# Optimization experiments

Hardware: AMD Instinct MI355X
Metric: run time of the kernel (lower is better)

Reference implementation:

```python
import math
import jax, jax.numpy as jnp
import numpy as np

N_NODES = 100000
N_EDGES = 1600000
IN_DIM, HID_DIM, OUT_DIM = 8, 64, 112


def _glorot(key, fan_in, fan_out):
    lim = math.sqrt(6.0 / (fan_in + fan_out))
    return jax.random.uniform(key, (fan_in, fan_out), jnp.float32, -lim, lim)


def _layer_params(key, in_d, out_d):
    ks = jax.random.split(key, 8)
    return dict(
        Wq=_glorot(ks[0], in_d, out_d), bq=jnp.zeros((out_d,), jnp.float32),
        Wk=_glorot(ks[1], in_d, out_d), bk=jnp.zeros((out_d,), jnp.float32),
        Wv=_glorot(ks[2], in_d, out_d), bv=jnp.zeros((out_d,), jnp.float32),
        Ws=_glorot(ks[3], in_d, out_d), bs=jnp.zeros((out_d,), jnp.float32),
    )


def setup_inputs() -> dict:
    key = jax.random.key(0)
    kx, ke, k0, k1, k2 = jax.random.split(key, 5)
    inp = {
        'x': jax.random.normal(kx, (N_NODES, IN_DIM), jnp.float32),
        'edge_index': jax.random.randint(ke, (2, N_EDGES), 0, N_NODES, jnp.int64),
    }
    for li, (kk, ind, outd) in enumerate([(k0, IN_DIM, HID_DIM), (k1, HID_DIM, HID_DIM), (k2, HID_DIM, OUT_DIM)]):
        p = _layer_params(kk, ind, outd)
        for name, v in p.items():
            inp[f'{name}{li}'] = v
    return inp


def _transformer_conv(x, src, dst, Wq, bq, Wk, bk, Wv, bv, Ws, bs):
    # heads=1, concat=True, no edge_attr, eval mode (no dropout)
    N = x.shape[0]
    C = Wq.shape[1]
    q = x @ Wq + bq            # [N, C]
    k = x @ Wk + bk
    v = x @ Wv + bv
    # per-edge attention score: <q_dst, k_src> / sqrt(C)
    scores = jnp.sum(q[dst] * k[src], axis=-1) * (1.0 / math.sqrt(C))  # [E]
    # segment softmax over destination neighborhoods (stable)
    m = jax.ops.segment_max(scores, dst, num_segments=N)               # [N]
    e = jnp.exp(scores - m[dst])                                       # [E]
    denom = jax.ops.segment_sum(e, dst, num_segments=N)                # [N]
    alpha = e / denom[dst]                                             # [E]
    # weighted scatter-add of source values to destinations
    out = jax.ops.segment_sum(alpha[:, None] * v[src], dst, num_segments=N)  # [N, C]
    # root/skip connection
    return out + (x @ Ws + bs)


def reference(x, edge_index,
              Wq0, bq0, Wk0, bk0, Wv0, bv0, Ws0, bs0,
              Wq1, bq1, Wk1, bk1, Wv1, bv1, Ws1, bs1,
              Wq2, bq2, Wk2, bk2, Wv2, bv2, Ws2, bs2):
    src, dst = edge_index[0], edge_index[1]
    h = _transformer_conv(x, src, dst, Wq0, bq0, Wk0, bk0, Wv0, bv0, Ws0, bs0)
    h = jax.nn.relu(h)
    h = _transformer_conv(h, src, dst, Wq1, bq1, Wk1, bk1, Wv1, bv1, Ws1, bs1)
    h = jax.nn.relu(h)
    out = _transformer_conv(h, src, dst, Wq2, bq2, Wk2, bk2, Wv2, bv2, Ws2, bs2)
    return out
```

## Files before the change

### kernel.cpp

```cpp
#include <hip/hip_runtime.h>
#include <hip/hip_fp16.h>
#include <math.h>
#include <float.h>
#include <stdint.h>

#define NN 100000
#define NE 1600000

#define SCAN_T 256
#define SCAN_E 1024
#define SCAN_NB ((NN + SCAN_E - 1) / SCAN_E)

#define NBUCK ((NN + 255) / 256)
#define EPB   4096
#define NBLK  ((NE + EPB - 1) / EPB)
#define HISTN (NBUCK * NBLK)
#define GS_NB ((HISTN + SCAN_E - 1) / SCAN_E)
#define BCAP  5120

typedef __attribute__((ext_vector_type(8))) short short8v;
typedef __attribute__((ext_vector_type(4))) float float4v;

__device__ __forceinline__ unsigned short f32_to_bf16_rne(float f) {
    unsigned u = __float_as_uint(f);
    u += 0x7FFFu + ((u >> 16) & 1u);
    return (unsigned short)(u >> 16);
}
__device__ __forceinline__ float bf16_to_f32(unsigned short h) {
    return __uint_as_float(((unsigned)h) << 16);
}

template<int K, int OUT>
__global__ __launch_bounds__(256)
void prep_w(const float* __restrict__ Wq, const float* __restrict__ Wk,
            const float* __restrict__ Wv, const float* __restrict__ Ws,
            unsigned short* __restrict__ wsp) {
    constexpr int NKS  = (K + 31) / 32;
    constexpr int OUTT = 4 * OUT;
    constexpr int NCT  = OUTT / 16;
    int idx = blockIdx.x * 256 + threadIdx.x;
    if (idx >= NCT * NKS * 512) return;
    int j    = idx & 7;
    int lane = (idx >> 3) & 63;
    int cell = idx >> 9;
    int ks   = cell % NKS;
    int ct   = cell / NKS;
    int g = lane >> 4, ln = lane & 15;
    int k = ks * 32 + g * 8 + j;
    int c = ct * 16 + ln;
    int mat = c / OUT, cm = c % OUT;
    const float* W = (mat == 0) ? Wq : (mat == 1) ? Wk : (mat == 2) ? Wv : Ws;
    float f = (k < K) ? W[(size_t)k * OUT + cm] : 0.f;
    unsigned short h = f32_to_bf16_rne(f);
    float resid = f - bf16_to_f32(h);
    wsp[(size_t)cell * 1024 + lane * 8 + j]       = h;
    wsp[(size_t)cell * 1024 + 512 + lane * 8 + j] = f32_to_bf16_rne(resid);
}

template<int K, int OUT, int CTSPLIT>
__global__ __launch_bounds__(256)
void gemm_qkvs(const float* __restrict__ x,
               const unsigned short* __restrict__ wsp,
               const float* __restrict__ bq, const float* __restrict__ bk,
               const float* __restrict__ bv, const float* __restrict__ bs,
               float* __restrict__ q, unsigned short* __restrict__ kv,
               float* __restrict__ outskip) {
    constexpr int NKS  = (K + 31) / 32;
    constexpr int OUTT = 4 * OUT;
    constexpr int NCT  = OUTT / 16;
    constexpr int CTPB = NCT / CTSPLIT;

    const int t    = threadIdx.x;
    const int lane = t & 63;
    const int wv   = t >> 6;
    const int g    = lane >> 4;
    const int ln   = lane & 15;
    const int rowbase = (blockIdx.x * 4 + wv) * 32;
    if (rowbase >= NN) return;

    union F8 { short8v v; unsigned short s[8]; uint4 u4; };

    F8 ahi[2][NKS], alo[2][NKS];
#pragma unroll
    for (int rt = 0; rt < 2; ++rt) {
        int r = rowbase + rt * 16 + ln;
        if (r >= NN) r = NN - 1;
        const float* rowp = x + (size_t)r * K;
#pragma unroll
        for (int ks = 0; ks < NKS; ++ks) {
            const int k0 = ks * 32 + g * 8;
            float xv[8];
            if (k0 + 8 <= K) {
                float4 p0 = *(const float4*)(rowp + k0);
                float4 p1 = *(const float4*)(rowp + k0 + 4);
                xv[0] = p0.x; xv[1] = p0.y; xv[2] = p0.z; xv[3] = p0.w;
                xv[4] = p1.x; xv[5] = p1.y; xv[6] = p1.z; xv[7] = p1.w;
            } else {
#pragma unroll
                for (int j = 0; j < 8; ++j) xv[j] = 0.f;
            }
#pragma unroll
            for (int j = 0; j < 8; ++j) {
                unsigned short h = f32_to_bf16_rne(xv[j]);
                ahi[rt][ks].s[j] = h;
                alo[rt][ks].s[j] = f32_to_bf16_rne(xv[j] - bf16_to_f32(h));
            }
        }
    }

    const int ct0 = blockIdx.y * CTPB;
#pragma unroll 1
    for (int ct = ct0; ct < ct0 + CTPB; ++ct) {
        F8 bhi[NKS], blo[NKS];
        const unsigned short* wp = wsp + (size_t)(ct * NKS) * 1024 + lane * 8;
#pragma unroll
        for (int ks = 0; ks < NKS; ++ks) {
            bhi[ks].u4 = *(const uint4*)(wp + ks * 1024);
            blo[ks].u4 = *(const uint4*)(wp + ks * 1024 + 512);
        }

        const int cb  = ct * 16;
        const int mat = cb / OUT;
        const int cm  = (cb % OUT) + ln;
        const float* B = (mat == 0) ? bq : (mat == 1) ? bk : (mat == 2) ? bv : bs;
        const float bias = B[cm];
        float4v acc0 = {bias, bias, bias, bias};
        float4v acc1 = {bias, bias, bias, bias};
#pragma unroll
        for (int ks = 0; ks < NKS; ++ks) {
            acc0 = __builtin_amdgcn_mfma_f32_16x16x32_bf16(ahi[0][ks].v, blo[ks].v, acc0, 0, 0, 0);
            acc0 = __builtin_amdgcn_mfma_f32_16x16x32_bf16(alo[0][ks].v, bhi[ks].v, acc0, 0, 0, 0);
            acc0 = __builtin_amdgcn_mfma_f32_16x16x32_bf16(ahi[0][ks].v, bhi[ks].v, acc0, 0, 0, 0);
            acc1 = __builtin_amdgcn_mfma_f32_16x16x32_bf16(ahi[1][ks].v, blo[ks].v, acc1, 0, 0, 0);
            acc1 = __builtin_amdgcn_mfma_f32_16x16x32_bf16(alo[1][ks].v, bhi[ks].v, acc1, 0, 0, 0);
            acc1 = __builtin_amdgcn_mfma_f32_16x16x32_bf16(ahi[1][ks].v, bhi[ks].v, acc1, 0, 0, 0);
        }

        if (mat == 0 || mat == 3) {
            float* dst = (mat == 0) ? q : outskip;
#pragma unroll
            for (int rt = 0; rt < 2; ++rt) {
                float4v a = rt ? acc1 : acc0;
#pragma unroll
                for (int reg = 0; reg < 4; ++reg) {
                    int node = rowbase + rt * 16 + g * 4 + reg;
                    if (node < NN)
                        dst[(size_t)node * OUT + cm] = a[reg];
                }
            }
        } else {
            const int base = (mat == 1) ? 0 : 4;
            const int kvoff = ((cm >> 2) * 8) + (cm & 3) + base;
#pragma unroll
            for (int rt = 0; rt < 2; ++rt) {
                float4v a = rt ? acc1 : acc0;
#pragma unroll
                for (int reg = 0; reg < 4; ++reg) {
                    int node = rowbase + rt * 16 + g * 4 + reg;
                    float f = a[reg];
                    float other = __shfl_xor(f, 1);
                    if (node < NN && !(ln & 1)) {
                        unsigned lo16 = __half_as_ushort(__float2half_rn(f));
                        unsigned hi16 = __half_as_ushort(__float2half_rn(other));
                        *(unsigned*)(kv + (size_t)node * (2 * OUT) + kvoff)
                            = lo16 | (hi16 << 16);
                    }
                }
            }
        }
    }
}

__global__ __launch_bounds__(256)
void bin_count(const int* __restrict__ ei, int* __restrict__ hist) {
    __shared__ int h[NBUCK];
    const int t = threadIdx.x;
    for (int i = t; i < NBUCK; i += 256) h[i] = 0;
    __syncthreads();
    int e0 = blockIdx.x * EPB;
    int e1 = e0 + EPB < NE ? e0 + EPB : NE;
    for (int i = e0 + t; i < e1; i += 256)
        atomicAdd(&h[ei[NE + i] >> 8], 1);
    __syncthreads();
    for (int i = t; i < NBUCK; i += 256)
        hist[(size_t)i * NBLK + blockIdx.x] = h[i];
}

__global__ __launch_bounds__(SCAN_T)
void gscan1(int* __restrict__ a, int* __restrict__ bsums) {
    __shared__ int lds[SCAN_T];
    int t = threadIdx.x;
    int base = blockIdx.x * SCAN_E + t * 4;
    int vals[4];
    int s = 0;
#pragma unroll
    for (int j = 0; j < 4; ++j) {
        int idx = base + j;
        vals[j] = (idx < HISTN) ? a[idx] : 0;
        s += vals[j];
    }
    lds[t] = s;
    __syncthreads();
    for (int off = 1; off < SCAN_T; off <<= 1) {
        int xx = (t >= off) ? lds[t - off] : 0;
        __syncthreads();
        lds[t] += xx;
        __syncthreads();
    }
    int run = (t > 0) ? lds[t - 1] : 0;
    if (t == SCAN_T - 1) bsums[blockIdx.x] = lds[t];
#pragma unroll
    for (int j = 0; j < 4; ++j) {
        int idx = base + j;
        if (idx < HISTN) a[idx] = run;
        run += vals[j];
    }
}

__global__ __launch_bounds__(256)
void gscan2(int* __restrict__ bsums) {
    __shared__ int lds[256];
    int t = threadIdx.x;
    lds[t] = (t < GS_NB) ? bsums[t] : 0;
    __syncthreads();
    for (int off = 1; off < 256; off <<= 1) {
        int xx = (t >= off) ? lds[t - off] : 0;
        __syncthreads();
        lds[t] += xx;
        __syncthreads();
    }
    if (t < GS_NB) bsums[t] = (t > 0) ? lds[t - 1] : 0;
}

__global__ __launch_bounds__(256)
void gscan3(int* __restrict__ a, const int* __restrict__ bsums,
            int* __restrict__ bstart) {
    int i = blockIdx.x * 256 + threadIdx.x;
    if (i < HISTN) {
        int v = a[i] + bsums[i / SCAN_E];
        a[i] = v;
        if (i % NBLK == 0) bstart[i / NBLK] = v;
    }
    if (i == 0) bstart[NBUCK] = NE;
}

__global__ __launch_bounds__(256)
void bin_scatter(const int* __restrict__ ei, const int* __restrict__ hist,
                 unsigned* __restrict__ ebuf) {
    __shared__ int off[NBUCK];
    const int t = threadIdx.x;
    for (int i = t; i < NBUCK; i += 256)
        off[i] = hist[(size_t)i * NBLK + blockIdx.x];
    __syncthreads();
    int e0 = blockIdx.x * EPB;
    int e1 = e0 + EPB < NE ? e0 + EPB : NE;
    for (int i = e0 + t; i < e1; i += 256) {
        int src = ei[i];
        int dst = ei[NE + i];
        int b = dst >> 8;
        int p = atomicAdd(&off[b], 1);
        ebuf[p] = ((unsigned)(dst & 255) << 17) | (unsigned)src;
    }
}

__global__ __launch_bounds__(256)
void bucket_hist(const int* __restrict__ bstart,
                 const unsigned* __restrict__ ebuf,
                 int* __restrict__ counts) {
    __shared__ int h[256];
    const int b = blockIdx.x;
    const int t = threadIdx.x;
    h[t] = 0;
    __syncthreads();
    int beg = bstart[b], end = bstart[b + 1];
    for (int i = beg + t; i < end; i += 256)
        atomicAdd(&h[ebuf[i] >> 17], 1);
    __syncthreads();
    int d = b * 256 + t;
    if (d < NN) counts[d] = h[t];
}

__global__ __launch_bounds__(SCAN_T)
void scan1(const int* __restrict__ counts, int* __restrict__ offsets,
           int* __restrict__ blocksums) {
    __shared__ int lds[SCAN_T];
    int t = threadIdx.x;
    int base = blockIdx.x * SCAN_E + t * 4;
    int vals[4];
    int s = 0;
#pragma unroll
    for (int j = 0; j < 4; ++j) {
        int idx = base + j;
        vals[j] = (idx < NN) ? counts[idx] : 0;
        s += vals[j];
    }
    lds[t] = s;
    __syncthreads();
    for (int off = 1; off < SCAN_T; off <<= 1) {
        int xx = (t >= off) ? lds[t - off] : 0;
        __syncthreads();
        lds[t] += xx;
        __syncthreads();
    }
    int run = (t > 0) ? lds[t - 1] : 0;
    if (t == SCAN_T - 1) blocksums[blockIdx.x] = lds[t];
#pragma unroll
    for (int j = 0; j < 4; ++j) {
        int idx = base + j;
        if (idx < NN) offsets[idx] = run;
        run += vals[j];
    }
}

__global__ __launch_bounds__(128)
void scan2(int* __restrict__ blocksums) {
    __shared__ int lds[128];
    int t = threadIdx.x;
    lds[t] = (t < SCAN_NB) ? blocksums[t] : 0;
    __syncthreads();
    for (int off = 1; off < 128; off <<= 1) {
        int xx = (t >= off) ? lds[t - off] : 0;
        __syncthreads();
        lds[t] += xx;
        __syncthreads();
    }
    if (t < SCAN_NB) blocksums[t] = (t > 0) ? lds[t - 1] : 0;
}

__global__ __launch_bounds__(256)
void scan3(int* __restrict__ offsets, const int* __restrict__ blocksums) {
    int i = blockIdx.x * blockDim.x + threadIdx.x;
    if (i < NN) offsets[i] = offsets[i] + blocksums[i / SCAN_E];
    if (i == 0) offsets[NN] = NE;
}

__global__ __launch_bounds__(256)
void csr_write(const int* __restrict__ bstart,
               const unsigned* __restrict__ ebuf,
               const int* __restrict__ offsets,
               int* __restrict__ sorted_src) {
    __shared__ int h[256];
    __shared__ int pre[256];
    __shared__ int posi[256];
    __shared__ unsigned srt[BCAP];
    const int b = blockIdx.x;
    const int t = threadIdx.x;
    h[t] = 0;
    __syncthreads();
    int beg = bstart[b];
    int cnt = bstart[b + 1] - beg;
    cnt = cnt < BCAP ? cnt : BCAP;
    const unsigned* buf = ebuf + beg;
    for (int i = t; i < cnt; i += 256)
        atomicAdd(&h[buf[i] >> 17], 1);
    __syncthreads();
    int v = h[t];
    pre[t] = v;
    __syncthreads();
    for (int off = 1; off < 256; off <<= 1) {
        int xx = (t >= off) ? pre[t - off] : 0;
        __syncthreads();
        pre[t] += xx;
        __syncthreads();
    }
    posi[t] = pre[t] - v;
    __syncthreads();
    for (int i = t; i < cnt; i += 256) {
        unsigned u = buf[i];
        int dl = u >> 17;
        int p = atomicAdd(&posi[dl], 1);
        srt[p] = u & 0x1FFFFu;
    }
    __syncthreads();
    const int base = offsets[b << 8];
    for (int i = t; i < cnt; i += 256)
        sorted_src[base + i] = (int)srt[i];
}

__device__ __forceinline__ float row16_sum(float x) {
    int y;
    y = __builtin_amdgcn_update_dpp(0, __float_as_int(x), 0x121, 0xF, 0xF, true); x += __int_as_float(y);
    y = __builtin_amdgcn_update_dpp(0, __float_as_int(x), 0x122, 0xF, 0xF, true); x += __int_as_float(y);
    y = __builtin_amdgcn_update_dpp(0, __float_as_int(x), 0x124, 0xF, 0xF, true); x += __int_as_float(y);
    y = __builtin_amdgcn_update_dpp(0, __float_as_int(x), 0x128, 0xF, 0xF, true); x += __int_as_float(y);
    return x;
}

__device__ __forceinline__ float4 h4_to_f4(unsigned wx, unsigned wy) {
    union { unsigned u; __half2 h; } a, b;
    a.u = wx; b.u = wy;
    float2 f0 = __half22float2(a.h);
    float2 f1 = __half22float2(b.h);
    return make_float4(f0.x, f0.y, f1.x, f1.y);
}

template<int C, bool RELU>
__global__ __launch_bounds__(256)
void attn_gather(const int* __restrict__ offsets,
                 const int* __restrict__ sorted_src,
                 const float* __restrict__ q,
                 const unsigned short* __restrict__ kv,
                 float* __restrict__ out, float scale) {
    const int wid  = (int)((blockIdx.x * blockDim.x + threadIdx.x) >> 6);
    const int lane = threadIdx.x & 63;
    if (wid >= NN) return;
    const int grp = lane >> 4;
    const int ch  = (lane & 15) * 4;
    constexpr bool P2 = (C > 64);
    const bool hi = P2 && (ch + 64 < C);

    const int beg = offsets[wid], end = offsets[wid + 1];

    const float sl = scale * 1.44269504f;
    float4 qv0 = *(const float4*)(q + (size_t)wid * C + ch);
    qv0.x *= sl; qv0.y *= sl; qv0.z *= sl; qv0.w *= sl;
    float4 qv1 = make_float4(0.f, 0.f, 0.f, 0.f);
    if (hi) {
        qv1 = *(const float4*)(q + (size_t)wid * C + ch + 64);
        qv1.x *= sl; qv1.y *= sl; qv1.z *= sl; qv1.w *= sl;
    }

    float m = -FLT_MAX, l = 0.f;
    float4 a0 = make_float4(0.f, 0.f, 0.f, 0.f);
    float4 a1 = make_float4(0.f, 0.f, 0.f, 0.f);

    const uint4 zz = make_uint4(0, 0, 0, 0);
    uint4 A0 = zz, A1 = zz, B0 = zz, B1 = zz;

    int i = beg + grp;
    if (i < end) {
        const unsigned short* row = kv + (size_t)sorted_src[i] * (2 * C);
        A0 = *(const uint4*)(row + 2 * ch);
        if (hi) A1 = *(const uint4*)(row + 2 * ch + 128);
    }
    if (i + 4 < end) {
        const unsigned short* row = kv + (size_t)sorted_src[i + 4] * (2 * C);
        B0 = *(const uint4*)(row + 2 * ch);
        if (hi) B1 = *(const uint4*)(row + 2 * ch + 128);
    }

    while (i < end) {
        uint4 N0 = zz, N1 = zz;
        int ip = i + 8;
        if (ip < end) {
            const unsigned short* row = kv + (size_t)sorted_src[ip] * (2 * C);
            N0 = *(const uint4*)(row + 2 * ch);
            if (hi) N1 = *(const uint4*)(row + 2 * ch + 128);
        }
        float4 kf0 = h4_to_f4(A0.x, A0.y);
        float4 vf0 = h4_to_f4(A0.z, A0.w);
        float part = qv0.x * kf0.x + qv0.y * kf0.y + qv0.z * kf0.z + qv0.w * kf0.w;
        float4 vf1 = make_float4(0.f, 0.f, 0.f, 0.f);
        if (P2) {
            float4 kf1 = h4_to_f4(A1.x, A1.y);
            vf1 = h4_to_f4(A1.z, A1.w);
            part += qv1.x * kf1.x + qv1.y * kf1.y + qv1.z * kf1.z + qv1.w * kf1.w;
        }
        float s = row16_sum(part);
        float mn = fmaxf(m, s);
        float al = __builtin_amdgcn_exp2f(m - mn);
        float w  = __builtin_amdgcn_exp2f(s - mn);
        l = l * al + w;
        a0.x = a0.x * al + w * vf0.x; a0.y = a0.y * al + w * vf0.y;
        a0.z = a0.z * al + w * vf0.z; a0.w = a0.w * al + w * vf0.w;
        if (P2) {
            a1.x = a1.x * al + w * vf1.x; a1.y = a1.y * al + w * vf1.y;
            a1.z = a1.z * al + w * vf1.z; a1.w = a1.w * al + w * vf1.w;
        }
        m = mn;
        A0 = B0; A1 = B1; B0 = N0; B1 = N1;
        i += 4;
    }

#pragma unroll
    for (int d = 16; d <= 32; d <<= 1) {
        float mo = __shfl_xor(m, d);
        float lo = __shfl_xor(l, d);
        float4 ao0, ao1;
        ao0.x = __shfl_xor(a0.x, d); ao0.y = __shfl_xor(a0.y, d);
        ao0.z = __shfl_xor(a0.z, d); ao0.w = __shfl_xor(a0.w, d);
        if (P2) {
            ao1.x = __shfl_xor(a1.x, d); ao1.y = __shfl_xor(a1.y, d);
            ao1.z = __shfl_xor(a1.z, d); ao1.w = __shfl_xor(a1.w, d);
        }
        float mn = fmaxf(m, mo);
        float e1 = (l  > 0.f) ? __builtin_amdgcn_exp2f(m  - mn) : 0.f;
        float e2 = (lo > 0.f) ? __builtin_amdgcn_exp2f(mo - mn) : 0.f;
        l = l * e1 + lo * e2;
        a0.x = a0.x * e1 + ao0.x * e2; a0.y = a0.y * e1 + ao0.y * e2;
        a0.z = a0.z * e1 + ao0.z * e2; a0.w = a0.w * e1 + ao0.w * e2;
        if (P2) {
            a1.x = a1.x * e1 + ao1.x * e2; a1.y = a1.y * e1 + ao1.y * e2;
            a1.z = a1.z * e1 + ao1.z * e2; a1.w = a1.w * e1 + ao1.w * e2;
        }
        m = mn;
    }

    if (lane < 16) {
        float inv = (l > 0.f) ? 1.f / l : 0.f;
        size_t o = (size_t)wid * C + ch;
        float4 sk = *(const float4*)(out + o);
        float4 r;
        r.x = sk.x + a0.x * inv; r.y = sk.y + a0.y * inv;
        r.z = sk.z + a0.z * inv; r.w = sk.w + a0.w * inv;
        if (RELU) {
            r.x = fmaxf(r.x, 0.f); r.y = fmaxf(r.y, 0.f);
            r.z = fmaxf(r.z, 0.f); r.w = fmaxf(r.w, 0.f);
        }
        *(float4*)(out + o) = r;
        if (hi) {
            float4 sk1 = *(const float4*)(out + o + 64);
            float4 r1;
            r1.x = sk1.x + a1.x * inv; r1.y = sk1.y + a1.y * inv;
            r1.z = sk1.z + a1.z * inv; r1.w = sk1.w + a1.w * inv;
            if (RELU) {
                r1.x = fmaxf(r1.x, 0.f); r1.y = fmaxf(r1.y, 0.f);
                r1.z = fmaxf(r1.z, 0.f); r1.w = fmaxf(r1.w, 0.f);
            }
            *(float4*)(out + o + 64) = r1;
        }
    }
}

template<int K, int OUT, bool RELU>
static void run_layer(const float* xin, const unsigned short* wsp,
                      const float* const* Wb,
                      const int* offsets, const int* sorted_src,
                      float* q, unsigned short* kv,
                      float* out, hipStream_t stream) {
    constexpr int CTSPLIT = 2;
    dim3 gg((NN + 127) / 128, CTSPLIT);
    gemm_qkvs<K, OUT, CTSPLIT><<<gg, 256, 0, stream>>>(
        xin, wsp, Wb[1], Wb[3], Wb[5], Wb[7], q, kv, out);

    float scale = 1.0f / sqrtf((float)OUT);
    attn_gather<OUT, RELU><<<(NN + 3) / 4, 256, 0, stream>>>(
        offsets, sorted_src, q, kv, out, scale);
}

extern "C" void kernel_launch(void* const* d_in, const int* in_sizes, int n_in,
                              void* d_out, int out_size, void* d_ws, size_t ws_size,
                              hipStream_t stream) {
    const float* x  = (const float*)d_in[0];
    const int*   ei = (const int*)d_in[1];
    const float* Wb0[8], *Wb1[8], *Wb2[8];
    for (int i = 0; i < 8; ++i) {
        Wb0[i] = (const float*)d_in[2 + i];
        Wb1[i] = (const float*)d_in[10 + i];
        Wb2[i] = (const float*)d_in[18 + i];
    }
    float* out = (float*)d_out;

    char* ws = (char*)d_ws;
    const size_t CMAX = 112;
    size_t off = 0;
    float*          q  = (float*)(ws + off);          off += (size_t)NN * CMAX * 4;
    unsigned short* kv = (unsigned short*)(ws + off); off += (size_t)NN * 2 * CMAX * 2;
    float* h0          = (float*)(ws + off);          off += (size_t)NN * 64 * 4;
    float* h1          = (float*)(ws + off);          off += (size_t)NN * 64 * 4;
    int*   sorted_src  = (int*)(ws + off);            off += (size_t)NE * 4;
    int*   counts      = (int*)(ws + off);            off += (size_t)NN * 4;
    int*   offsets     = (int*)(ws + off);            off += (size_t)(NN + 1) * 4;
    int*   blocksums   = (int*)(ws + off);            off += (size_t)SCAN_NB * 4;
    int*   hist        = (int*)(ws + off);            off += (size_t)HISTN * 4;
    int*   gsums       = (int*)(ws + off);            off += (size_t)GS_NB * 4;
    int*   bstart      = (int*)(ws + off);            off += (size_t)(NBUCK + 1) * 4;
    unsigned* ebuf     = (unsigned*)(ws + off);       off += (size_t)NE * 4;
    (void)ws_size; (void)in_sizes; (void)n_in; (void)out_size;

    bin_count<<<NBLK, 256, 0, stream>>>(ei, hist);
    gscan1<<<GS_NB, SCAN_T, 0, stream>>>(hist, gsums);
    gscan2<<<1, 256, 0, stream>>>(gsums);
    gscan3<<<(HISTN + 255) / 256, 256, 0, stream>>>(hist, gsums, bstart);
    bin_scatter<<<NBLK, 256, 0, stream>>>(ei, hist, ebuf);
    bucket_hist<<<NBUCK, 256, 0, stream>>>(bstart, ebuf, counts);
    scan1<<<SCAN_NB, SCAN_T, 0, stream>>>(counts, offsets, blocksums);
    scan2<<<1, 128, 0, stream>>>(blocksums);
    scan3<<<(NN + 255) / 256, 256, 0, stream>>>(offsets, blocksums);
    csr_write<<<NBUCK, 256, 0, stream>>>(bstart, ebuf, offsets, sorted_src);

    unsigned short* wspbase =
        (unsigned short*)(((uintptr_t)ebuf + 255) & ~(uintptr_t)255);
    unsigned short* wsp0 = wspbase;
    unsigned short* wsp1 = wsp0 + 16 * 1 * 1024;
    unsigned short* wsp2 = wsp1 + 16 * 2 * 1024;
    prep_w<8, 64><<<(16 * 1 * 512 + 255) / 256, 256, 0, stream>>>(
        Wb0[0], Wb0[2], Wb0[4], Wb0[6], wsp0);
    prep_w<64, 64><<<(16 * 2 * 512 + 255) / 256, 256, 0, stream>>>(
        Wb1[0], Wb1[2], Wb1[4], Wb1[6], wsp1);
    prep_w<64, 112><<<(28 * 2 * 512 + 255) / 256, 256, 0, stream>>>(
        Wb2[0], Wb2[2], Wb2[4], Wb2[6], wsp2);

    run_layer<8,  64, true >(x,  wsp0, Wb0, offsets, sorted_src, q, kv, h0,  stream);
    run_layer<64, 64, true >(h0, wsp1, Wb1, offsets, sorted_src, q, kv, h1,  stream);
    run_layer<64, 112, false>(h1, wsp2, Wb2, offsets, sorted_src, q, kv, out, stream);
}
```

Measured before the change: 551.7 us.

## Process eight edges per wave in attention gather with 8-lane groups

Reworks the attention gather kernel so each wave handles 8 edges at once, using 8-lane groups of 8 channels each, instead of 4 edges with 16-lane groups of 4 channels. The dot-product reduction shrinks to a 3-step DPP/swizzle sum, and the prefetch pipeline is restructured as an unrolled A/B double buffer. The aim is more memory-level parallelism per wave on the random neighbour gathers and fewer cross-lane reduction steps per edge. In exchange each lane holds more registers (16 accumulators plus up to 8 uint4 buffers), which may reduce occupancy, and the final cross-group merge needs an extra shuffle round.

```diff
diff --git a/kernel.cpp b/kernel.cpp
--- a/kernel.cpp
+++ b/kernel.cpp
@@ -377,21 +377,23 @@
         sorted_src[base + i] = (int)srt[i];
 }
 
-__device__ __forceinline__ float row16_sum(float x) {
+__device__ __forceinline__ float grp8_sum(float x) {
     int y;
-    y = __builtin_amdgcn_update_dpp(0, __float_as_int(x), 0x121, 0xF, 0xF, true); x += __int_as_float(y);
-    y = __builtin_amdgcn_update_dpp(0, __float_as_int(x), 0x122, 0xF, 0xF, true); x += __int_as_float(y);
-    y = __builtin_amdgcn_update_dpp(0, __float_as_int(x), 0x124, 0xF, 0xF, true); x += __int_as_float(y);
-    y = __builtin_amdgcn_update_dpp(0, __float_as_int(x), 0x128, 0xF, 0xF, true); x += __int_as_float(y);
+    y = __builtin_amdgcn_update_dpp(0, __float_as_int(x), 0xB1, 0xF, 0xF, true); x += __int_as_float(y);
+    y = __builtin_amdgcn_update_dpp(0, __float_as_int(x), 0x4E, 0xF, 0xF, true); x += __int_as_float(y);
+    y = __builtin_amdgcn_ds_swizzle(__float_as_int(x), 0x101F);                  x += __int_as_float(y);
     return x;
 }
 
-__device__ __forceinline__ float4 h4_to_f4(unsigned wx, unsigned wy) {
-    union { unsigned u; __half2 h; } a, b;
-    a.u = wx; b.u = wy;
-    float2 f0 = __half22float2(a.h);
-    float2 f1 = __half22float2(b.h);
-    return make_float4(f0.x, f0.y, f1.x, f1.y);
+__device__ __forceinline__ float d2(float acc, unsigned kk, float q0, float q1) {
+    float2 f = __half22float2(*(__half2*)&kk);
+    acc = fmaf(f.x, q0, acc);
+    return fmaf(f.y, q1, acc);
+}
+__device__ __forceinline__ void upd2(float& a0, float& a1, unsigned vv, float al, float w) {
+    float2 f = __half22float2(*(__half2*)&vv);
+    a0 = fmaf(a0, al, w * f.x);
+    a1 = fmaf(a1, al, w * f.y);
 }
 
 template<int C, bool RELU>
@@ -404,120 +406,151 @@
     const int wid  = (int)((blockIdx.x * blockDim.x + threadIdx.x) >> 6);
     const int lane = threadIdx.x & 63;
     if (wid >= NN) return;
-    const int grp = lane >> 4;
-    const int ch  = (lane & 15) * 4;
-    constexpr bool P2 = (C > 64);
-    const bool hi = P2 && (ch + 64 < C);
+    const int grp = lane >> 3;
+    const int sub = lane & 7;
+    constexpr bool P2  = (C > 64);
+    constexpr int NAV  = P2 ? 16 : 8;
+    const bool hi = P2 && (sub < (C - 64) / 8);
 
     const int beg = offsets[wid], end = offsets[wid + 1];
-
     const float sl = scale * 1.44269504f;
-    float4 qv0 = *(const float4*)(q + (size_t)wid * C + ch);
-    qv0.x *= sl; qv0.y *= sl; qv0.z *= sl; qv0.w *= sl;
-    float4 qv1 = make_float4(0.f, 0.f, 0.f, 0.f);
-    if (hi) {
-        qv1 = *(const float4*)(q + (size_t)wid * C + ch + 64);
-        qv1.x *= sl; qv1.y *= sl; qv1.z *= sl; qv1.w *= sl;
+
+    const float* qrow = q + (size_t)wid * C + sub * 8;
+    float qf[NAV];
+    {
+        float4 q0 = *(const float4*)(qrow);
+        float4 q1 = *(const float4*)(qrow + 4);
+        qf[0] = q0.x * sl; qf[1] = q0.y * sl; qf[2] = q0.z * sl; qf[3] = q0.w * sl;
+        qf[4] = q1.x * sl; qf[5] = q1.y * sl; qf[6] = q1.z * sl; qf[7] = q1.w * sl;
+        if (P2) {
+#pragma unroll
+            for (int j = 8; j < NAV; ++j) qf[j] = 0.f;
+            if (hi) {
+                float4 q2 = *(const float4*)(qrow + 64);
+                float4 q3 = *(const float4*)(qrow + 68);
+                qf[8]  = q2.x * sl; qf[9]  = q2.y * sl; qf[10] = q2.z * sl; qf[11] = q2.w * sl;
+                qf[12] = q3.x * sl; qf[13] = q3.y * sl; qf[14] = q3.z * sl; qf[15] = q3.w * sl;
+            }
+        }
     }
 
     float m = -FLT_MAX, l = 0.f;
-    float4 a0 = make_float4(0.f, 0.f, 0.f, 0.f);
-    float4 a1 = make_float4(0.f, 0.f, 0.f, 0.f);
+    float av[NAV];
+#pragma unroll
+    for (int j = 0; j < NAV; ++j) av[j] = 0.f;
 
     const uint4 zz = make_uint4(0, 0, 0, 0);
-    uint4 A0 = zz, A1 = zz, B0 = zz, B1 = zz;
+    uint4 A0 = zz, A1 = zz, A2 = zz, A3 = zz;
+    uint4 B0 = zz, B1 = zz, B2 = zz, B3 = zz;
+
+#define GLOAD(S0, S1, S2, S3, IDX)                                            \
+    if ((IDX) < end) {                                                        \
+        const unsigned short* row_ =                                          \
+            kv + (size_t)sorted_src[IDX] * (2 * C) + 16 * sub;                \
+        S0 = *(const uint4*)(row_);                                           \
+        S1 = *(const uint4*)(row_ + 8);                                       \
+        if (P2 && hi) {                                                       \
+            S2 = *(const uint4*)(row_ + 128);                                 \
+            S3 = *(const uint4*)(row_ + 136);                                 \
+        }                                                                     \
+    }
+
+#define GCOMP(S0, S1, S2, S3)                                                 \
+    {                                                                         \
+        float part = 0.f;                                                     \
+        part = d2(part, S0.x, qf[0], qf[1]);                                  \
+        part = d2(part, S0.y, qf[2], qf[3]);                                  \
+        part = d2(part, S1.x, qf[4], qf[5]);                                  \
+        part = d2(part, S1.y, qf[6], qf[7]);                                  \
+        if (P2) {                                                             \
+            part = d2(part, S2.x, qf[8],  qf[9]);                             \
+            part = d2(part, S2.y, qf[10], qf[11]);                            \
+            part = d2(part, S3.x, qf[12], qf[13]);                            \
+            part = d2(part, S3.y, qf[14], qf[15]);                            \
+        }                                                                     \
+        float s  = grp8_sum(part);                                            \
+        float mn = fmaxf(m, s);                                               \
+        float al = __builtin_amdgcn_exp2f(m - mn);                            \
+        float w  = __builtin_amdgcn_exp2f(s - mn);                            \
+        l = l * al + w;                                                       \
+        upd2(av[0], av[1], S0.z, al, w);                                      \
+        upd2(av[2], av[3], S0.w, al, w);                                      \
+        upd2(av[4], av[5], S1.z, al, w);                                      \
+        upd2(av[6], av[7], S1.w, al, w);                                      \
+        if (P2) {                                                             \
+            upd2(av[8],  av[9],  S2.z, al, w);                                \
+            upd2(av[10], av[11], S2.w, al, w);                                \
+            upd2(av[12], av[13], S3.z, al, w);                                \
+            upd2(av[14], av[15], S3.w, al, w);                                \
+        }                                                                     \
+        m = mn;                                                               \
+    }
 
     int i = beg + grp;
-    if (i < end) {
-        const unsigned short* row = kv + (size_t)sorted_src[i] * (2 * C);
-        A0 = *(const uint4*)(row + 2 * ch);
-        if (hi) A1 = *(const uint4*)(row + 2 * ch + 128);
-    }
-    if (i + 4 < end) {
-        const unsigned short* row = kv + (size_t)sorted_src[i + 4] * (2 * C);
-        B0 = *(const uint4*)(row + 2 * ch);
-        if (hi) B1 = *(const uint4*)(row + 2 * ch + 128);
-    }
-
+    GLOAD(A0, A1, A2, A3, i)
+    GLOAD(B0, B1, B2, B3, i + 8)
     while (i < end) {
-        uint4 N0 = zz, N1 = zz;
-        int ip = i + 8;
-        if (ip < end) {
-            const unsigned short* row = kv + (size_t)sorted_src[ip] * (2 * C);
-            N0 = *(const uint4*)(row + 2 * ch);
-            if (hi) N1 = *(const uint4*)(row + 2 * ch + 128);
-        }
-        float4 kf0 = h4_to_f4(A0.x, A0.y);
-        float4 vf0 = h4_to_f4(A0.z, A0.w);
-        float part = qv0.x * kf0.x + qv0.y * kf0.y + qv0.z * kf0.z + qv0.w * kf0.w;
-        float4 vf1 = make_float4(0.f, 0.f, 0.f, 0.f);
-        if (P2) {
-            float4 kf1 = h4_to_f4(A1.x, A1.y);
-            vf1 = h4_to_f4(A1.z, A1.w);
-            part += qv1.x * kf1.x + qv1.y * kf1.y + qv1.z * kf1.z + qv1.w * kf1.w;
-        }
-        float s = row16_sum(part);
-        float mn = fmaxf(m, s);
-        float al = __builtin_amdgcn_exp2f(m - mn);
-        float w  = __builtin_amdgcn_exp2f(s - mn);
-        l = l * al + w;
-        a0.x = a0.x * al + w * vf0.x; a0.y = a0.y * al + w * vf0.y;
-        a0.z = a0.z * al + w * vf0.z; a0.w = a0.w * al + w * vf0.w;
-        if (P2) {
-            a1.x = a1.x * al + w * vf1.x; a1.y = a1.y * al + w * vf1.y;
-            a1.z = a1.z * al + w * vf1.z; a1.w = a1.w * al + w * vf1.w;
-        }
-        m = mn;
-        A0 = B0; A1 = B1; B0 = N0; B1 = N1;
-        i += 4;
-    }
-
-#pragma unroll
-    for (int d = 16; d <= 32; d <<= 1) {
+        GCOMP(A0, A1, A2, A3)
+        GLOAD(A0, A1, A2, A3, i + 16)
+        i += 8;
+        if (i >= end) break;
+        GCOMP(B0, B1, B2, B3)
+        GLOAD(B0, B1, B2, B3, i + 16)
+        i += 8;
+    }
+#undef GLOAD
+#undef GCOMP
+
+#pragma unroll
+    for (int d = 8; d <= 32; d <<= 1) {
         float mo = __shfl_xor(m, d);
         float lo = __shfl_xor(l, d);
-        float4 ao0, ao1;
-        ao0.x = __shfl_xor(a0.x, d); ao0.y = __shfl_xor(a0.y, d);
-        ao0.z = __shfl_xor(a0.z, d); ao0.w = __shfl_xor(a0.w, d);
-        if (P2) {
-            ao1.x = __shfl_xor(a1.x, d); ao1.y = __shfl_xor(a1.y, d);
-            ao1.z = __shfl_xor(a1.z, d); ao1.w = __shfl_xor(a1.w, d);
-        }
         float mn = fmaxf(m, mo);
         float e1 = (l  > 0.f) ? __builtin_amdgcn_exp2f(m  - mn) : 0.f;
         float e2 = (lo > 0.f) ? __builtin_amdgcn_exp2f(mo - mn) : 0.f;
         l = l * e1 + lo * e2;
-        a0.x = a0.x * e1 + ao0.x * e2; a0.y = a0.y * e1 + ao0.y * e2;
-        a0.z = a0.z * e1 + ao0.z * e2; a0.w = a0.w * e1 + ao0.w * e2;
-        if (P2) {
-            a1.x = a1.x * e1 + ao1.x * e2; a1.y = a1.y * e1 + ao1.y * e2;
-            a1.z = a1.z * e1 + ao1.z * e2; a1.w = a1.w * e1 + ao1.w * e2;
+#pragma unroll
+        for (int j = 0; j < NAV; ++j) {
+            float ao = __shfl_xor(av[j], d);
+            av[j] = av[j] * e1 + ao * e2;
         }
         m = mn;
     }
 
-    if (lane < 16) {
+    if (grp == 0) {
         float inv = (l > 0.f) ? 1.f / l : 0.f;
-        size_t o = (size_t)wid * C + ch;
-        float4 sk = *(const float4*)(out + o);
-        float4 r;
-        r.x = sk.x + a0.x * inv; r.y = sk.y + a0.y * inv;
-        r.z = sk.z + a0.z * inv; r.w = sk.w + a0.w * inv;
+        size_t o = (size_t)wid * C + sub * 8;
+        float4 s0 = *(const float4*)(out + o);
+        float4 s1 = *(const float4*)(out + o + 4);
+        float4 r0, r1;
+        r0.x = s0.x + av[0] * inv; r0.y = s0.y + av[1] * inv;
+        r0.z = s0.z + av[2] * inv; r0.w = s0.w + av[3] * inv;
+        r1.x = s1.x + av[4] * inv; r1.y = s1.y + av[5] * inv;
+        r1.z = s1.z + av[6] * inv; r1.w = s1.w + av[7] * inv;
         if (RELU) {
-            r.x = fmaxf(r.x, 0.f); r.y = fmaxf(r.y, 0.f);
-            r.z = fmaxf(r.z, 0.f); r.w = fmaxf(r.w, 0.f);
-        }
-        *(float4*)(out + o) = r;
-        if (hi) {
-            float4 sk1 = *(const float4*)(out + o + 64);
-            float4 r1;
-            r1.x = sk1.x + a1.x * inv; r1.y = sk1.y + a1.y * inv;
-            r1.z = sk1.z + a1.z * inv; r1.w = sk1.w + a1.w * inv;
+            r0.x = fmaxf(r0.x, 0.f); r0.y = fmaxf(r0.y, 0.f);
+            r0.z = fmaxf(r0.z, 0.f); r0.w = fmaxf(r0.w, 0.f);
+            r1.x = fmaxf(r1.x, 0.f); r1.y = fmaxf(r1.y, 0.f);
+            r1.z = fmaxf(r1.z, 0.f); r1.w = fmaxf(r1.w, 0.f);
+        }
+        *(float4*)(out + o)     = r0;
+        *(float4*)(out + o + 4) = r1;
+        if (P2 && hi) {
+            float4 s2 = *(const float4*)(out + o + 64);
+            float4 s3 = *(const float4*)(out + o + 68);
+            float4 r2, r3;
+            r2.x = s2.x + av[8]  * inv; r2.y = s2.y + av[9]  * inv;
+            r2.z = s2.z + av[10] * inv; r2.w = s2.w + av[11] * inv;
+            r3.x = s3.x + av[12] * inv; r3.y = s3.y + av[13] * inv;
+            r3.z = s3.z + av[14] * inv; r3.w = s3.w + av[15] * inv;
             if (RELU) {
-                r1.x = fmaxf(r1.x, 0.f); r1.y = fmaxf(r1.y, 0.f);
-                r1.z = fmaxf(r1.z, 0.f); r1.w = fmaxf(r1.w, 0.f);
+                r2.x = fmaxf(r2.x, 0.f); r2.y = fmaxf(r2.y, 0.f);
+                r2.z = fmaxf(r2.z, 0.f); r2.w = fmaxf(r2.w, 0.f);
+                r3.x = fmaxf(r3.x, 0.f); r3.y = fmaxf(r3.y, 0.f);
+                r3.z = fmaxf(r3.z, 0.f); r3.w = fmaxf(r3.w, 0.f);
             }
-            *(float4*)(out + o + 64) = r1;
+            *(float4*)(out + o + 64) = r2;
+            *(float4*)(out + o + 68) = r3;
         }
     }
 }
```

Result: no change. 562.5 us (+2.0%).
